# Kernel optimization log

Hardware: AMD Instinct MI355X
Metric: run time of the kernel (lower is better)

Reference implementation:

```python
import jax, jax.numpy as jnp
import numpy as np

NEG_SLOPE = 0.2
EPS = 1e-16  # PyG softmax eps


def gat_conv(x, src, dst, W, a_src, a_dst, bias, heads, out_dim, concat):
    """PyG GATConv (shared lin for src/dst, self-loops already appended).
    x: (N, in), W: (heads*out, in), a_src/a_dst: (heads, out), bias matches output.
    """
    N = x.shape[0]
    h = (x @ W.T).reshape(N, heads, out_dim)            # (N, H, D)
    alpha_s = jnp.sum(h * a_src[None], axis=-1)          # (N, H)
    alpha_d = jnp.sum(h * a_dst[None], axis=-1)          # (N, H)
    e = jax.nn.leaky_relu(alpha_s[src] + alpha_d[dst], NEG_SLOPE)  # (E, H)
    # segment softmax over destination node (self-loops guarantee nonempty segments)
    m = jax.ops.segment_max(e, dst, num_segments=N)      # (N, H)
    ex = jnp.exp(e - m[dst])
    s = jax.ops.segment_sum(ex, dst, num_segments=N)     # (N, H)
    alpha = ex / (s[dst] + EPS)                          # (E, H)
    msg = h[src] * alpha[:, :, None]                     # (E, H, D)
    out = jax.ops.segment_sum(msg, dst, num_segments=N)  # (N, H, D)
    if concat:
        out = out.reshape(N, heads * out_dim)
    else:
        out = out.mean(axis=1)
    return out + bias


def setup_inputs() -> dict:
    key = jax.random.key(0)
    ks = jax.random.split(key, 12)
    N, E, in_dim, hid, heads = 50000, 800000, 256, 64, 4
    sc1 = 1.0 / np.sqrt(in_dim)
    sc2 = 1.0 / np.sqrt(hid * heads)
    return {
        "x": jax.random.normal(ks[0], (N, in_dim), dtype=jnp.float32),
        "edge_index": jax.random.randint(ks[1], (2, E), 0, N, dtype=jnp.int32),
        "W1": jax.random.normal(ks[2], (heads * hid, in_dim), dtype=jnp.float32) * sc1,
        "a_src1": jax.random.normal(ks[3], (heads, hid), dtype=jnp.float32) * sc1,
        "a_dst1": jax.random.normal(ks[4], (heads, hid), dtype=jnp.float32) * sc1,
        "b1": jnp.zeros((heads * hid,), dtype=jnp.float32),
        "W2": jax.random.normal(ks[5], (hid, heads * hid), dtype=jnp.float32) * sc2,
        "a_src2": jax.random.normal(ks[6], (1, hid), dtype=jnp.float32) * sc2,
        "a_dst2": jax.random.normal(ks[7], (1, hid), dtype=jnp.float32) * sc2,
        "b2": jnp.zeros((hid,), dtype=jnp.float32),
    }


def reference(x, edge_index, W1, a_src1, a_dst1, b1, W2, a_src2, a_dst2, b2):
    N = x.shape[0]
    loops = jnp.arange(N, dtype=edge_index.dtype)
    src = jnp.concatenate([edge_index[0], loops])
    dst = jnp.concatenate([edge_index[1], loops])
    h = gat_conv(x, src, dst, W1, a_src1, a_dst1, b1, heads=4, out_dim=64, concat=True)
    h = jax.nn.elu(h)
    out = gat_conv(h, src, dst, W2, a_src2, a_dst2, b2, heads=1, out_dim=64, concat=False)
    return out
```

## Files before the change

### kernel.cpp

```cpp
#include <hip/hip_runtime.h>
#include <hip/hip_bf16.h>


#define NEG_SLOPE 0.2f
#define SM_EPS 1e-16f

typedef unsigned short u16;
typedef unsigned int u32;
typedef __attribute__((ext_vector_type(8))) short short8v;
typedef __attribute__((ext_vector_type(4))) float f32x4;
typedef __attribute__((ext_vector_type(2))) float f32x2;

__device__ __forceinline__ float bf2f(u16 u) { return __uint_as_float(((u32)u) << 16); }
__device__ __forceinline__ u16 f2bf(float f) {
  u32 u = __float_as_uint(f);
  u = (u + 0x7FFFu + ((u >> 16) & 1u)) >> 16;
  return (u16)u;
}
__device__ __forceinline__ float lrelu(float e) { return e > 0.f ? e : NEG_SLOPE * e; }
__device__ __forceinline__ f32x2 bfpair(u32 p) {
  f32x2 r;
  r.x = __uint_as_float(p << 16);
  r.y = __uint_as_float(p & 0xFFFF0000u);
  return r;
}

template <int BN, int WGM, int WGN, int ABF16, int HEADS>
__global__ __launch_bounds__(256, 2) void gemm_mfma(const void* __restrict__ Av,
                                                    const float* __restrict__ B,
                                                    u16* __restrict__ C,
                                                    const float* __restrict__ a_src,
                                                    const float* __restrict__ a_dst,
                                                    float* __restrict__ as_out,
                                                    float* __restrict__ ad_out, int M) {
  constexpr int K = 256, BK = 64, BM = 64;
  constexpr int WM = BM / WGM, WN = BN / WGN;
  constexpr int MF = WM / 16, NF = WN / 16;
  __shared__ short lds[(BM + BN) * BK];
  short* Al = lds;
  short* Bl = lds + BM * BK;
  const int t = threadIdx.x;
  const int wid = t >> 6, lane = t & 63;
  const int wm = wid / WGN, wn = wid % WGN;
  const int row0 = blockIdx.x * BM;
  const int l15 = lane & 15, l4 = lane >> 4;
  f32x4 acc[MF][NF] = {};
  for (int k0 = 0; k0 < K; k0 += BK) {
    for (int g = t; g < BM * 8; g += 256) {
      int row = g >> 3, c = g & 7;
      int gr = row0 + row;
      short8v v;
      if (ABF16) {
        if (gr < M)
          v = *reinterpret_cast<const short8v*>((const short*)Av + (size_t)gr * K + k0 + c * 8);
        else
          v = (short8v)(short)0;
      } else {
        if (gr < M) {
          const float* ap = (const float*)Av + (size_t)gr * K + k0 + c * 8;
          float4 f0 = *reinterpret_cast<const float4*>(ap);
          float4 f1 = *reinterpret_cast<const float4*>(ap + 4);
          v[0] = (short)f2bf(f0.x); v[1] = (short)f2bf(f0.y);
          v[2] = (short)f2bf(f0.z); v[3] = (short)f2bf(f0.w);
          v[4] = (short)f2bf(f1.x); v[5] = (short)f2bf(f1.y);
          v[6] = (short)f2bf(f1.z); v[7] = (short)f2bf(f1.w);
        } else {
          v = (short8v)(short)0;
        }
      }
      *reinterpret_cast<short8v*>(&Al[row * BK + ((c * 8) ^ ((row & 7) << 3))]) = v;
    }
    for (int g = t; g < BN * 8; g += 256) {
      int row = g >> 3, c = g & 7;
      const float* bp = B + (size_t)row * K + k0 + c * 8;
      float4 f0 = *reinterpret_cast<const float4*>(bp);
      float4 f1 = *reinterpret_cast<const float4*>(bp + 4);
      short8v v;
      v[0] = (short)f2bf(f0.x); v[1] = (short)f2bf(f0.y);
      v[2] = (short)f2bf(f0.z); v[3] = (short)f2bf(f0.w);
      v[4] = (short)f2bf(f1.x); v[5] = (short)f2bf(f1.y);
      v[6] = (short)f2bf(f1.z); v[7] = (short)f2bf(f1.w);
      *reinterpret_cast<short8v*>(&Bl[row * BK + ((c * 8) ^ ((row & 7) << 3))]) = v;
    }
    __syncthreads();
#pragma unroll
    for (int ks = 0; ks < BK / 32; ++ks) {
      short8v af[MF], bfr[NF];
#pragma unroll
      for (int fm = 0; fm < MF; ++fm) {
        int row = wm * WM + fm * 16 + l15;
        int col = (ks * 32 + l4 * 8) ^ ((row & 7) << 3);
        af[fm] = *reinterpret_cast<const short8v*>(&Al[row * BK + col]);
      }
#pragma unroll
      for (int fn = 0; fn < NF; ++fn) {
        int row = wn * WN + fn * 16 + l15;
        int col = (ks * 32 + l4 * 8) ^ ((row & 7) << 3);
        bfr[fn] = *reinterpret_cast<const short8v*>(&Bl[row * BK + col]);
      }
#pragma unroll
      for (int fm = 0; fm < MF; ++fm)
#pragma unroll
        for (int fn = 0; fn < NF; ++fn)
          acc[fm][fn] =
              __builtin_amdgcn_mfma_f32_16x16x32_bf16(af[fm], bfr[fn], acc[fm][fn], 0, 0, 0);
    }
    __syncthreads();
  }
#pragma unroll
  for (int fm = 0; fm < MF; ++fm) {
#pragma unroll
    for (int fn = 0; fn < NF; ++fn) {
      int r0 = row0 + wm * WM + fm * 16 + l4 * 4;
      int col = wn * WN + fn * 16 + l15;
#pragma unroll
      for (int r = 0; r < 4; ++r)
        if (r0 + r < M) C[(size_t)(r0 + r) * BN + col] = f2bf(acc[fm][fn][r]);
    }
  }
  float asv[NF], adv[NF];
#pragma unroll
  for (int fn = 0; fn < NF; ++fn) {
    asv[fn] = a_src[wn * WN + fn * 16 + l15];
    adv[fn] = a_dst[wn * WN + fn * 16 + l15];
  }
  if (HEADS == 4) {
#pragma unroll
    for (int fm = 0; fm < MF; ++fm) {
#pragma unroll
      for (int r = 0; r < 4; ++r) {
        float ps = 0.f, pd = 0.f;
#pragma unroll
        for (int fn = 0; fn < NF; ++fn) {
          ps = fmaf(acc[fm][fn][r], asv[fn], ps);
          pd = fmaf(acc[fm][fn][r], adv[fn], pd);
        }
#pragma unroll
        for (int off = 1; off < 16; off <<= 1) {
          ps += __shfl_xor(ps, off);
          pd += __shfl_xor(pd, off);
        }
        if (l15 == 0) {
          int row = row0 + wm * WM + fm * 16 + l4 * 4 + r;
          if (row < M) {
            as_out[(size_t)row * 4 + wn] = ps;
            ad_out[(size_t)row * 4 + wn] = pd;
          }
        }
      }
    }
  } else {
    float* redAs = (float*)lds;
    float* redAd = redAs + WGM * WGN * WM;
#pragma unroll
    for (int fm = 0; fm < MF; ++fm) {
#pragma unroll
      for (int r = 0; r < 4; ++r) {
        float ps = 0.f, pd = 0.f;
#pragma unroll
        for (int fn = 0; fn < NF; ++fn) {
          ps = fmaf(acc[fm][fn][r], asv[fn], ps);
          pd = fmaf(acc[fm][fn][r], adv[fn], pd);
        }
#pragma unroll
        for (int off = 1; off < 16; off <<= 1) {
          ps += __shfl_xor(ps, off);
          pd += __shfl_xor(pd, off);
        }
        if (l15 == 0) {
          int rl = fm * 16 + l4 * 4 + r;
          redAs[(wm * WGN + wn) * WM + rl] = ps;
          redAd[(wm * WGN + wn) * WM + rl] = pd;
        }
      }
    }
    __syncthreads();
    if (t < BM) {
      int wmx = t / WM, rl = t % WM;
      float s = 0.f, d = 0.f;
      for (int w = 0; w < WGN; ++w) {
        s += redAs[(wmx * WGN + w) * WM + rl];
        d += redAd[(wmx * WGN + w) * WM + rl];
      }
      int row = row0 + t;
      if (row < M) {
        as_out[row] = s;
        ad_out[row] = d;
      }
    }
  }
}

__global__ void count_kernel(const int* __restrict__ ei, int E, int N,
                             int* __restrict__ counts, int* __restrict__ rank) {
  int e = blockIdx.x * blockDim.x + threadIdx.x;
  if (e >= E + N) return;
  int d = (e < E) ? ei[E + e] : (e - E);
  rank[e] = atomicAdd(&counts[d], 1);
}

__global__ __launch_bounds__(256) void blocksum_kernel(const int* __restrict__ counts,
                                                       int* __restrict__ bsums, int N) {
  const int b = blockIdx.x, t = threadIdx.x;
  const int base = b * 1024 + t * 4;
  int s = 0;
#pragma unroll
  for (int i = 0; i < 4; ++i) {
    int idx = base + i;
    if (idx < N) s += counts[idx];
  }
#pragma unroll
  for (int off = 1; off < 64; off <<= 1) s += __shfl_xor(s, off);
  __shared__ int ws[4];
  if ((t & 63) == 0) ws[t >> 6] = s;
  __syncthreads();
  if (t == 0) bsums[b] = ws[0] + ws[1] + ws[2] + ws[3];
}

__global__ __launch_bounds__(256) void scanfinal_kernel(const int* __restrict__ counts,
                                                        const int* __restrict__ bsums,
                                                        int* __restrict__ rowptr,
                                                        int N, int nb) {
  const int b = blockIdx.x, t = threadIdx.x;
  const int wave = t >> 6, lane = t & 63;
  __shared__ int boff_s;
  if (t < 64) {
    int s = 0;
    for (int base = 0; base < nb; base += 64) {
      int i = base + lane;
      s += (i < nb && i < b) ? bsums[i] : 0;
    }
#pragma unroll
    for (int off = 1; off < 64; off <<= 1) s += __shfl_xor(s, off);
    if (lane == 0) boff_s = s;
  }
  const int base = b * 1024 + t * 4;
  int v[4];
#pragma unroll
  for (int i = 0; i < 4; ++i) {
    int idx = base + i;
    v[i] = (idx < N) ? counts[idx] : 0;
  }
  int ts = v[0] + v[1] + v[2] + v[3];
  int inc = ts;
#pragma unroll
  for (int off = 1; off < 64; off <<= 1) {
    int u = __shfl_up(inc, off);
    if (lane >= off) inc += u;
  }
  __shared__ int wsum[4];
  if (lane == 63) wsum[wave] = inc;
  __syncthreads();
  int woff = 0;
  for (int w = 0; w < 4; ++w)
    if (w < wave) woff += wsum[w];
  int run = boff_s + woff + (inc - ts);
#pragma unroll
  for (int i = 0; i < 4; ++i) {
    int idx = base + i;
    if (idx < N) rowptr[idx] = run;
    run += v[i];
  }
  if (N - 1 >= base && N - 1 < base + 4) rowptr[N] = run;
}

__global__ void scatter_kernel(const int* __restrict__ ei, int E, int N,
                               const int* __restrict__ rowptr, const int* __restrict__ rank,
                               int* __restrict__ srcs) {
  int e = blockIdx.x * blockDim.x + threadIdx.x;
  if (e >= E + N) return;
  int s = (e < E) ? ei[e] : (e - E);
  int d = (e < E) ? ei[E + e] : (e - E);
  srcs[rowptr[d] + rank[e]] = s;
}

__global__ __launch_bounds__(256) void gather1_kernel(const u16* __restrict__ h1b,
                                                      const int* __restrict__ rowptr,
                                                      const int* __restrict__ srcs,
                                                      const float* __restrict__ as1,
                                                      const float* __restrict__ ad1,
                                                      const float* __restrict__ b1,
                                                      u16* __restrict__ act1b, int N) {
  const int wave = threadIdx.x >> 6, lane = threadIdx.x & 63;
  const int n = blockIdx.x * 4 + wave;
  if (n >= N) return;
  const int h = lane >> 4, l15 = lane & 15;
  const int beg = rowptr[n], end = rowptr[n + 1];
  const int deg = end - beg;
  const float ad = ad1[(size_t)n * 4 + h];
  float ev[4];
  int sr[4];
  float m = -1e30f;
#pragma unroll
  for (int c = 0; c < 4; ++c) {
    int idx = c * 16 + l15;
    bool ok = idx < deg;
    int si = ok ? srcs[beg + idx] : 0;
    sr[c] = si;
    float e = ok ? lrelu(as1[(size_t)si * 4 + h] + ad) : -1e30f;
    ev[c] = e;
    m = fmaxf(m, e);
  }
  for (int j0 = beg + 64; j0 < end; j0 += 16) {
    int j = j0 + l15;
    if (j < end) m = fmaxf(m, lrelu(as1[(size_t)srcs[j] * 4 + h] + ad));
  }
#pragma unroll
  for (int off = 1; off < 16; off <<= 1) m = fmaxf(m, __shfl_xor(m, off));
  float s = 0.f;
#pragma unroll
  for (int c = 0; c < 4; ++c) {
    ev[c] = __expf(ev[c] - m);
    s += ev[c];
  }
  for (int j0 = beg + 64; j0 < end; j0 += 16) {
    int j = j0 + l15;
    if (j < end) s += __expf(lrelu(as1[(size_t)srcs[j] * 4 + h] + ad) - m);
  }
#pragma unroll
  for (int off = 1; off < 16; off <<= 1) s += __shfl_xor(s, off);
  const float rs = 1.f / (s + SM_EPS);
#pragma unroll
  for (int c = 0; c < 4; ++c) ev[c] *= rs;
  f32x2 a01 = (f32x2)(0.f), a23 = (f32x2)(0.f);
  const u32* h1w = reinterpret_cast<const u32*>(h1b);
  const int lim = deg < 64 ? deg : 64;
#pragma unroll
  for (int c = 0; c < 4; ++c) {
    const int base = c * 16;
    if (base < lim) {
      int cnt = lim - base;
      if (cnt > 16) cnt = 16;
      if (cnt == 16) {
#pragma unroll
        for (int k = 0; k < 16; ++k) {
          float wk = __shfl(ev[c], h * 16 + k);
          int sk = __shfl(sr[c], h * 16 + k);
          uint2 v = *reinterpret_cast<const uint2*>(&h1w[(size_t)sk * 128 + lane * 2]);
          f32x2 w2 = {wk, wk};
          a01 += w2 * bfpair(v.x);
          a23 += w2 * bfpair(v.y);
        }
      } else {
        for (int k = 0; k < cnt; ++k) {
          float wk = __shfl(ev[c], h * 16 + k);
          int sk = __shfl(sr[c], h * 16 + k);
          uint2 v = *reinterpret_cast<const uint2*>(&h1w[(size_t)sk * 128 + lane * 2]);
          f32x2 w2 = {wk, wk};
          a01 += w2 * bfpair(v.x);
          a23 += w2 * bfpair(v.y);
        }
      }
    }
  }
  for (int j = beg + 64; j < end; ++j) {
    int si = srcs[j];
    float wk = __expf(lrelu(as1[(size_t)si * 4 + h] + ad) - m) * rs;
    uint2 v = *reinterpret_cast<const uint2*>(&h1w[(size_t)si * 128 + lane * 2]);
    f32x2 w2 = {wk, wk};
    a01 += w2 * bfpair(v.x);
    a23 += w2 * bfpair(v.y);
  }
  float4 bb = *reinterpret_cast<const float4*>(&b1[lane * 4]);
  float4 o;
  o.x = a01.x + bb.x; o.y = a01.y + bb.y; o.z = a23.x + bb.z; o.w = a23.y + bb.w;
  o.x = o.x > 0.f ? o.x : __expf(o.x) - 1.f;
  o.y = o.y > 0.f ? o.y : __expf(o.y) - 1.f;
  o.z = o.z > 0.f ? o.z : __expf(o.z) - 1.f;
  o.w = o.w > 0.f ? o.w : __expf(o.w) - 1.f;
  ushort4 ov;
  ov.x = f2bf(o.x); ov.y = f2bf(o.y); ov.z = f2bf(o.z); ov.w = f2bf(o.w);
  *reinterpret_cast<ushort4*>(&act1b[(size_t)n * 256 + lane * 4]) = ov;
}

__global__ __launch_bounds__(256) void gather2_kernel(const u16* __restrict__ h2b,
                                                      const int* __restrict__ rowptr,
                                                      const int* __restrict__ srcs,
                                                      const float* __restrict__ as2,
                                                      const float* __restrict__ ad2,
                                                      const float* __restrict__ b2,
                                                      float* __restrict__ out, int N) {
  const int wave = threadIdx.x >> 6, lane = threadIdx.x & 63;
  const int n = blockIdx.x * 4 + wave;
  if (n >= N) return;
  const int g = lane >> 4;
  const int c4 = (lane & 15) * 4;
  const int beg = rowptr[n], end = rowptr[n + 1];
  const int deg = end - beg;
  const float ad = ad2[n];
  bool ok = lane < deg;
  int si = ok ? srcs[beg + lane] : 0;
  float e = ok ? lrelu(as2[si] + ad) : -1e30f;
  float m = e;
  for (int j0 = beg + 64; j0 < end; j0 += 64) {
    int j = j0 + lane;
    if (j < end) m = fmaxf(m, lrelu(as2[srcs[j]] + ad));
  }
#pragma unroll
  for (int off = 1; off < 64; off <<= 1) m = fmaxf(m, __shfl_xor(m, off));
  float w = __expf(e - m);
  float s = w;
  for (int j0 = beg + 64; j0 < end; j0 += 64) {
    int j = j0 + lane;
    if (j < end) s += __expf(lrelu(as2[srcs[j]] + ad) - m);
  }
#pragma unroll
  for (int off = 1; off < 64; off <<= 1) s += __shfl_xor(s, off);
  const float rs = 1.f / (s + SM_EPS);
  w *= rs;
  f32x2 a01 = (f32x2)(0.f), a23 = (f32x2)(0.f);
  const u32* h2w = reinterpret_cast<const u32*>(h2b);
  const int lim = deg < 64 ? deg : 64;
  for (int j0 = 0; j0 < lim; j0 += 4) {
    int id = j0 + g;
    float wk = __shfl(w, id & 63);
    int sk = __shfl(si, id & 63);
    if (id >= lim) { wk = 0.f; sk = 0; }
    uint2 v = *reinterpret_cast<const uint2*>(&h2w[(size_t)sk * 32 + (c4 >> 1)]);
    f32x2 w2 = {wk, wk};
    a01 += w2 * bfpair(v.x);
    a23 += w2 * bfpair(v.y);
  }
  for (int j0 = beg + 64; j0 < end; j0 += 4) {
    int j = j0 + g;
    float wk = 0.f;
    int sk = 0;
    if (j < end) {
      sk = srcs[j];
      wk = __expf(lrelu(as2[sk] + ad) - m) * rs;
    }
    uint2 v = *reinterpret_cast<const uint2*>(&h2w[(size_t)sk * 32 + (c4 >> 1)]);
    f32x2 w2 = {wk, wk};
    a01 += w2 * bfpair(v.x);
    a23 += w2 * bfpair(v.y);
  }
  float4 acc = make_float4(a01.x, a01.y, a23.x, a23.y);
#pragma unroll
  for (int off = 16; off <= 32; off <<= 1) {
    acc.x += __shfl_xor(acc.x, off);
    acc.y += __shfl_xor(acc.y, off);
    acc.z += __shfl_xor(acc.z, off);
    acc.w += __shfl_xor(acc.w, off);
  }
  if (lane < 16) {
    float4 bb = *reinterpret_cast<const float4*>(&b2[c4]);
    float4 o = make_float4(acc.x + bb.x, acc.y + bb.y, acc.z + bb.z, acc.w + bb.w);
    *reinterpret_cast<float4*>(&out[(size_t)n * 64 + c4]) = o;
  }
}

extern "C" void kernel_launch(void* const* d_in, const int* in_sizes, int n_in,
                              void* d_out, int out_size, void* d_ws, size_t ws_size,
                              hipStream_t stream) {
  const float* x      = (const float*)d_in[0];
  const int*   ei     = (const int*)d_in[1];
  const float* W1     = (const float*)d_in[2];
  const float* a_src1 = (const float*)d_in[3];
  const float* a_dst1 = (const float*)d_in[4];
  const float* b1     = (const float*)d_in[5];
  const float* W2     = (const float*)d_in[6];
  const float* a_src2 = (const float*)d_in[7];
  const float* a_dst2 = (const float*)d_in[8];
  const float* b2     = (const float*)d_in[9];
  float* out = (float*)d_out;

  const int N = in_sizes[0] / 256;
  const int E = in_sizes[1] / 2;
  const int Etot = E + N;

  char* ws = (char*)d_ws;
  size_t off = 0;
  auto alloc = [&](size_t bytes) -> void* {
    off = (off + 255) & ~(size_t)255;
    void* p = ws + off;
    off += bytes;
    return p;
  };
  u16*   h1b    = (u16*)alloc((size_t)N * 256 * 2);
  u16*   act1b  = (u16*)alloc((size_t)N * 256 * 2);
  u16*   h2b    = (u16*)alloc((size_t)N * 64 * 2);
  float* as1    = (float*)alloc((size_t)N * 4 * 4);
  float* ad1    = (float*)alloc((size_t)N * 4 * 4);
  int*   counts = (int*)alloc((size_t)N * 4);
  int*   rowptr = (int*)alloc((size_t)(N + 1) * 4);
  int*   rank   = (int*)alloc((size_t)Etot * 4);
  int*   srcs   = (int*)alloc((size_t)Etot * 4);
  int*   bsums  = (int*)alloc((size_t)256 * 4);
  float* as2 = as1;
  float* ad2 = ad1;
  (void)ws_size; (void)n_in; (void)out_size;

  hipMemsetAsync(counts, 0, (size_t)N * 4, stream);
  int eblocks = (Etot + 255) / 256;
  count_kernel<<<eblocks, 256, 0, stream>>>(ei, E, N, counts, rank);
  const int nb = (N + 1023) / 1024;
  blocksum_kernel<<<nb, 256, 0, stream>>>(counts, bsums, N);
  scanfinal_kernel<<<nb, 256, 0, stream>>>(counts, bsums, rowptr, N, nb);
  scatter_kernel<<<eblocks, 256, 0, stream>>>(ei, E, N, rowptr, rank, srcs);

  const int gblocks = (N + 63) / 64;

  gemm_mfma<256, 1, 4, 0, 4><<<gblocks, 256, 0, stream>>>(x, W1, h1b, a_src1, a_dst1,
                                                          as1, ad1, N);
  gather1_kernel<<<(N + 3) / 4, 256, 0, stream>>>(h1b, rowptr, srcs, as1, ad1, b1, act1b, N);

  gemm_mfma<64, 2, 2, 1, 1><<<gblocks, 256, 0, stream>>>(act1b, W2, h2b, a_src2, a_dst2,
                                                         as2, ad2, N);
  gather2_kernel<<<(N + 3) / 4, 256, 0, stream>>>(h2b, rowptr, srcs, as2, ad2, b2, out, N);
}
```

Before: 207.7 us.

## Fuse degree counting into layer-1 GEMM launch and merge scan kernels

The edge degree-count atomics now run as extra blocks appended to the first GEMM grid, so counting overlaps the projection GEMM and needs no separate launch. The two-pass block-sum plus scan is replaced by one scan kernel in which each block recomputes its prefix offset by summing all earlier counts directly. This cuts two kernel launches and their serialization. In exchange, later blocks of the scan do redundant O(N) reads, and the atomic blocks contend with the GEMM blocks for compute units.

```diff
diff --git a/kernel.cpp b/kernel.cpp
--- a/kernel.cpp
+++ b/kernel.cpp
@@ -25,18 +25,29 @@
   return r;
 }
 
-template <int BN, int WGM, int WGN, int ABF16, int HEADS>
+template <int BN, int WGM, int WGN, int ABF16, int HEADS, int FUSE>
 __global__ __launch_bounds__(256, 2) void gemm_mfma(const void* __restrict__ Av,
                                                     const float* __restrict__ B,
                                                     u16* __restrict__ C,
                                                     const float* __restrict__ a_src,
                                                     const float* __restrict__ a_dst,
                                                     float* __restrict__ as_out,
-                                                    float* __restrict__ ad_out, int M) {
+                                                    float* __restrict__ ad_out, int M,
+                                                    const int* __restrict__ ei, int E,
+                                                    int* __restrict__ counts,
+                                                    int* __restrict__ rank, int gemmblocks) {
   constexpr int K = 256, BK = 64, BM = 64;
   constexpr int WM = BM / WGM, WN = BN / WGN;
   constexpr int MF = WM / 16, NF = WN / 16;
   __shared__ short lds[(BM + BN) * BK];
+  if (FUSE && blockIdx.x >= gemmblocks) {
+    int e = (blockIdx.x - gemmblocks) * 256 + threadIdx.x;
+    if (e < E + M) {
+      int d = (e < E) ? ei[E + e] : (e - E);
+      rank[e] = atomicAdd(&counts[d], 1);
+    }
+    return;
+  }
   short* Al = lds;
   short* Bl = lds + BM * BK;
   const int t = threadIdx.x;
@@ -191,49 +202,19 @@
   }
 }
 
-__global__ void count_kernel(const int* __restrict__ ei, int E, int N,
-                             int* __restrict__ counts, int* __restrict__ rank) {
-  int e = blockIdx.x * blockDim.x + threadIdx.x;
-  if (e >= E + N) return;
-  int d = (e < E) ? ei[E + e] : (e - E);
-  rank[e] = atomicAdd(&counts[d], 1);
-}
-
-__global__ __launch_bounds__(256) void blocksum_kernel(const int* __restrict__ counts,
-                                                       int* __restrict__ bsums, int N) {
-  const int b = blockIdx.x, t = threadIdx.x;
-  const int base = b * 1024 + t * 4;
-  int s = 0;
-#pragma unroll
-  for (int i = 0; i < 4; ++i) {
-    int idx = base + i;
-    if (idx < N) s += counts[idx];
-  }
-#pragma unroll
-  for (int off = 1; off < 64; off <<= 1) s += __shfl_xor(s, off);
-  __shared__ int ws[4];
-  if ((t & 63) == 0) ws[t >> 6] = s;
-  __syncthreads();
-  if (t == 0) bsums[b] = ws[0] + ws[1] + ws[2] + ws[3];
-}
-
-__global__ __launch_bounds__(256) void scanfinal_kernel(const int* __restrict__ counts,
-                                                        const int* __restrict__ bsums,
-                                                        int* __restrict__ rowptr,
-                                                        int N, int nb) {
+__global__ __launch_bounds__(256) void scanfused_kernel(const int* __restrict__ counts,
+                                                        int* __restrict__ rowptr, int N) {
   const int b = blockIdx.x, t = threadIdx.x;
   const int wave = t >> 6, lane = t & 63;
-  __shared__ int boff_s;
-  if (t < 64) {
-    int s = 0;
-    for (int base = 0; base < nb; base += 64) {
-      int i = base + lane;
-      s += (i < nb && i < b) ? bsums[i] : 0;
-    }
-#pragma unroll
-    for (int off = 1; off < 64; off <<= 1) s += __shfl_xor(s, off);
-    if (lane == 0) boff_s = s;
-  }
+  __shared__ int red[4];
+  int pre = 0;
+  for (int i = t; i < b * 1024; i += 256) pre += counts[i];
+#pragma unroll
+  for (int off = 1; off < 64; off <<= 1) pre += __shfl_xor(pre, off);
+  if (lane == 0) red[wave] = pre;
+  __syncthreads();
+  const int boff = red[0] + red[1] + red[2] + red[3];
+  __syncthreads();
   const int base = b * 1024 + t * 4;
   int v[4];
 #pragma unroll
@@ -254,7 +235,7 @@
   int woff = 0;
   for (int w = 0; w < 4; ++w)
     if (w < wave) woff += wsum[w];
-  int run = boff_s + woff + (inc - ts);
+  int run = boff + woff + (inc - ts);
 #pragma unroll
   for (int i = 0; i < 4; ++i) {
     int idx = base + i;
@@ -485,26 +466,25 @@
   int*   rowptr = (int*)alloc((size_t)(N + 1) * 4);
   int*   rank   = (int*)alloc((size_t)Etot * 4);
   int*   srcs   = (int*)alloc((size_t)Etot * 4);
-  int*   bsums  = (int*)alloc((size_t)256 * 4);
   float* as2 = as1;
   float* ad2 = ad1;
   (void)ws_size; (void)n_in; (void)out_size;
 
   hipMemsetAsync(counts, 0, (size_t)N * 4, stream);
-  int eblocks = (Etot + 255) / 256;
-  count_kernel<<<eblocks, 256, 0, stream>>>(ei, E, N, counts, rank);
+
+  const int eblocks = (Etot + 255) / 256;
+  const int gblocks = (N + 63) / 64;
   const int nb = (N + 1023) / 1024;
-  blocksum_kernel<<<nb, 256, 0, stream>>>(counts, bsums, N);
-  scanfinal_kernel<<<nb, 256, 0, stream>>>(counts, bsums, rowptr, N, nb);
+
+  gemm_mfma<256, 1, 4, 0, 4, 1><<<gblocks + eblocks, 256, 0, stream>>>(
+      x, W1, h1b, a_src1, a_dst1, as1, ad1, N, ei, E, counts, rank, gblocks);
+
+  scanfused_kernel<<<nb, 256, 0, stream>>>(counts, rowptr, N);
   scatter_kernel<<<eblocks, 256, 0, stream>>>(ei, E, N, rowptr, rank, srcs);
 
-  const int gblocks = (N + 63) / 64;
-
-  gemm_mfma<256, 1, 4, 0, 4><<<gblocks, 256, 0, stream>>>(x, W1, h1b, a_src1, a_dst1,
-                                                          as1, ad1, N);
   gather1_kernel<<<(N + 3) / 4, 256, 0, stream>>>(h1b, rowptr, srcs, as1, ad1, b1, act1b, N);
 
-  gemm_mfma<64, 2, 2, 1, 1><<<gblocks, 256, 0, stream>>>(act1b, W2, h2b, a_src2, a_dst2,
-                                                         as2, ad2, N);
+  gemm_mfma<64, 2, 2, 1, 1, 0><<<gblocks, 256, 0, stream>>>(
+      act1b, W2, h2b, a_src2, a_dst2, as2, ad2, N, nullptr, 0, nullptr, nullptr, gblocks);
   gather2_kernel<<<(N + 3) / 4, 256, 0, stream>>>(h2b, rowptr, srcs, as2, ad2, b2, out, N);
 }
```

After: 208.8 us. About the same (+0.5%).
